# Optimization experiments

Measured on AMD Instinct MI355X. Metric: run time of the kernel, lower is better.

The kernel has to match this reference:

```python
import jax, jax.numpy as jnp
import numpy as np

N = 100000      # nodes
E = 2500000     # edges
DIN, H, DOUT = 3, 32, 4
EPS = 1e-5

def _lin(k, i, o):
    kw, kb = jax.random.split(k)
    lim = 1.0 / np.sqrt(i)
    W = jax.random.uniform(kw, (i, o), jnp.float32, -lim, lim)
    b = jax.random.uniform(kb, (o,), jnp.float32, -lim, lim)
    return W, b

def setup_inputs():
    key = jax.random.key(0)
    ks = jax.random.split(key, 12)
    x = jax.random.normal(ks[0], (N, DIN), jnp.float32)
    edge_index = jax.random.randint(ks[1], (2, E), 0, N, dtype=jnp.int32)
    w_in1, b_in1 = _lin(ks[2], DIN, H)
    w_in2, b_in2 = _lin(ks[3], H, H)
    gamma = jnp.ones((H,), jnp.float32)
    beta = jnp.zeros((H,), jnp.float32)
    wg1, bg1 = _lin(ks[4], H, H)
    wg2, bg2 = _lin(ks[5], H, H)
    wg3, bg3 = _lin(ks[6], H, H)
    wo1, bo1 = _lin(ks[7], H, H)
    wo2, bo2 = _lin(ks[8], H, H)
    wo3, bo3 = _lin(ks[9], H, DOUT)
    return dict(x=x, w_in1=w_in1, b_in1=b_in1, w_in2=w_in2, b_in2=b_in2,
                gamma=gamma, beta=beta,
                wg1=wg1, bg1=bg1, wg2=wg2, bg2=bg2, wg3=wg3, bg3=bg3,
                wo1=wo1, bo1=bo1, wo2=wo2, bo2=bo2, wo3=wo3, bo3=bo3,
                edge_index=edge_index)

def _gcn(h, W, b, src, dst, norm):
    # PyG GCNConv: x' = scatter_add(norm * (xW)[src] -> dst) + bias
    hw = h @ W                                   # [N, H]
    msg = hw[src] * norm[:, None]                # [E+N, H] gather + scale
    out = jax.ops.segment_sum(msg, dst, num_segments=N)
    return out + b

def reference(x, w_in1, b_in1, w_in2, b_in2, gamma, beta,
              wg1, bg1, wg2, bg2, wg3, bg3,
              wo1, bo1, wo2, bo2, wo3, bo3, edge_index):
    leaky = lambda v: jax.nn.leaky_relu(v, 0.01)
    # input MLP
    h = leaky(x @ w_in1 + b_in1)
    h = leaky(h @ w_in2 + b_in2)
    # BatchNorm1d (training-mode batch statistics, biased variance)
    mu = jnp.mean(h, axis=0)
    var = jnp.mean((h - mu) ** 2, axis=0)
    h = (h - mu) * jax.lax.rsqrt(var + EPS) * gamma + beta
    # gcn_norm with self-loops: deg over target index, sym normalization
    loop = jnp.arange(N, dtype=edge_index.dtype)
    src = jnp.concatenate([edge_index[0], loop])
    dst = jnp.concatenate([edge_index[1], loop])
    deg = jax.ops.segment_sum(jnp.ones_like(src, jnp.float32), dst, num_segments=N)
    dis = jax.lax.rsqrt(deg)                     # deg >= 1 due to self-loops
    norm = dis[src] * dis[dst]                   # [E+N]
    h = jax.nn.elu(_gcn(h, wg1, bg1, src, dst, norm))
    h = jax.nn.elu(_gcn(h, wg2, bg2, src, dst, norm))
    h = jax.nn.elu(_gcn(h, wg3, bg3, src, dst, norm))
    # output MLP
    r = leaky(h @ wo1 + bo1)
    r = leaky(r @ wo2 + bo2)
    r = r @ wo3 + bo3                            # [N, 4]
    r = r.at[:, 0].set(jax.nn.sigmoid(r[:, 0]))
    return r
```

## Files before the change

### kernel.cpp

```cpp
#include <hip/hip_runtime.h>
#include <hip/hip_fp16.h>

#define HF 32
#define EPS 1e-5f
#define BSH 7
#define BSZ 128
#define CH  8192
#define SUBCAP 512
#define CAP (8*SUBCAP)

typedef int vi4 __attribute__((ext_vector_type(4)));

__device__ __forceinline__ float leaky(float v){ return fmaxf(v, 0.01f*v); }
__device__ __forceinline__ float elu1(float v){ return v > 0.f ? v : (expf(v)-1.f); }
__device__ __forceinline__ float sigmoidf(float v){ return 1.f/(1.f+expf(-v)); }

__device__ __forceinline__ int4 nt_load_i4(const int* p){
    vi4 v = __builtin_nontemporal_load((const vi4*)p);
    return make_int4(v.x, v.y, v.z, v.w);
}

__device__ __forceinline__ void addrow8(float* a, float4 v){
    const __half2* p = (const __half2*)&v;
#pragma unroll
    for (int k = 0; k < 4; k++){
        float2 f = __half22float2(p[k]);
        a[2*k] += f.x; a[2*k+1] += f.y;
    }
}
__device__ __forceinline__ float4 h2add4f(float4 a, float4 b){
    __half2* pa = (__half2*)&a; __half2* pb = (__half2*)&b;
    float4 r; __half2* pr = (__half2*)&r;
#pragma unroll
    for (int k = 0; k < 4; k++) pr[k] = __hadd2(pa[k], pb[k]);
    return r;
}

union SMem {
    struct {
        float sW1[3*HF]; float sB1[HF]; float sW2[HF*HF]; float sB2[HF];
        float sh[256][33];
    } mlp;
    struct { int lcnt[1024]; int lbase[1024]; int lpos[1024]; } bin;
};

__global__ __launch_bounds__(256)
void k_mlp_bin(const float* __restrict__ x,
               const float* __restrict__ w1, const float* __restrict__ b1,
               const float* __restrict__ w2, const float* __restrict__ b2,
               __half* __restrict__ h, float* __restrict__ stats,
               const int* __restrict__ src, const int* __restrict__ dst,
               int* __restrict__ gfill, int* __restrict__ ep,
               int N, int E, int B, int NB1){
    __shared__ SMem sm;
    int t = threadIdx.x;
    if ((int)blockIdx.x < NB1){
        for (int i = t; i < 3*HF; i += 256) sm.mlp.sW1[i] = w1[i];
        if (t < HF){ sm.mlp.sB1[t] = b1[t]; sm.mlp.sB2[t] = b2[t]; }
        for (int i = t; i < HF*HF; i += 256) sm.mlp.sW2[i] = w2[i];
        __syncthreads();
        int n = blockIdx.x*256 + t;
        float h2[HF];
        if (n < N){
            float x0 = x[(size_t)n*3], x1 = x[(size_t)n*3+1], x2 = x[(size_t)n*3+2];
            float h1[HF];
#pragma unroll
            for (int j = 0; j < HF; j++){
                float v = fmaf(x0, sm.mlp.sW1[j], fmaf(x1, sm.mlp.sW1[HF+j],
                          fmaf(x2, sm.mlp.sW1[2*HF+j], sm.mlp.sB1[j])));
                h1[j] = leaky(v);
            }
#pragma unroll
            for (int j = 0; j < HF; j++){
                float v = sm.mlp.sB2[j];
#pragma unroll
                for (int i = 0; i < HF; i++) v = fmaf(h1[i], sm.mlp.sW2[i*HF+j], v);
                h2[j] = leaky(v);
            }
            float4* hv = (float4*)(h + (size_t)n*HF);
#pragma unroll
            for (int jb = 0; jb < 4; jb++){
                __half2 hh[4];
#pragma unroll
                for (int k = 0; k < 4; k++)
                    hh[k] = __float22half2_rn(make_float2(h2[jb*8+2*k], h2[jb*8+2*k+1]));
                hv[jb] = *(float4*)hh;
            }
        } else {
#pragma unroll
            for (int j = 0; j < HF; j++) h2[j] = 0.f;
        }
#pragma unroll
        for (int j = 0; j < HF; j++) sm.mlp.sh[t][j] = h2[j];
        __syncthreads();
        int f = t & 31, g = t >> 5;
        float s = 0.f, ss = 0.f;
        for (int i = 0; i < 32; i++){
            float v = sm.mlp.sh[g*32 + i][f];
            s += v; ss += v*v;
        }
        __syncthreads();
        sm.mlp.sh[g][f] = s; sm.mlp.sh[8+g][f] = ss;
        __syncthreads();
        if (t < HF){
            float a = 0.f, b = 0.f;
#pragma unroll
            for (int g2 = 0; g2 < 8; g2++){ a += sm.mlp.sh[g2][t]; b += sm.mlp.sh[8+g2][t]; }
            atomicAdd(&stats[t], a);
            atomicAdd(&stats[HF+t], b);
        }
    } else {
        int bid = blockIdx.x - NB1;
        for (int i = t; i < B; i += 256){ sm.bin.lcnt[i] = 0; sm.bin.lpos[i] = 0; }
        __syncthreads();
        int base = bid * CH;
        int xcd = blockIdx.x & 7;
        int dv[16], sv[16];
        for (int half = 0; half < 2; half++){
            int hbase = base + half*4096;
#pragma unroll
            for (int i = 0; i < 16; i++){
                int e = hbase + t + i*256;
                dv[i] = (e < E) ? dst[e] : -1;
                sv[i] = (e < E) ? src[e] : 0;
            }
#pragma unroll
            for (int i = 0; i < 16; i++)
                if (dv[i] >= 0) atomicAdd(&sm.bin.lcnt[dv[i] >> BSH], 1);
            if (half == 0){
            }
            __syncthreads();
            if (half == 0){
            }
        }
        for (int i = t; i < B; i += 256){
            int c = sm.bin.lcnt[i];
            sm.bin.lbase[i] = c ? (i*CAP + xcd*SUBCAP + atomicAdd(&gfill[i*8 + xcd], c)) : 0;
        }
        __syncthreads();
        for (int half = 0; half < 2; half++){
            int hbase = base + half*4096;
#pragma unroll
            for (int i = 0; i < 16; i++){
                int e = hbase + t + i*256;
                if (e < E){
                    int d = dst[e], s = src[e];
                    int bb = d >> BSH;
                    int p = sm.bin.lbase[bb] + atomicAdd(&sm.bin.lpos[bb], 1);
                    ep[p] = (s << BSH) | (d & (BSZ-1));
                }
            }
        }
    }
}

__global__ __launch_bounds__(256)
void k_bucketD(int* __restrict__ ep, const int* __restrict__ gfill,
               int2* __restrict__ rowp2, float* __restrict__ dis, int N, int B){
    __shared__ int sep[CAP];
    __shared__ int lcnt[256], lpre[256], lfill[256], sc[256];
    int b = blockIdx.x, t = threadIdx.x;
    int cx[8], coff[8], cnt = 0;
#pragma unroll
    for (int x = 0; x < 8; x++){ cx[x] = gfill[b*8 + x]; coff[x] = cnt; cnt += cx[x]; }
    lcnt[t] = 0; lfill[t] = 0;
    __syncthreads();
    int base = b*CAP;
#pragma unroll
    for (int x = 0; x < 8; x++)
        for (int j = t; j < cx[x]; j += 256) sep[coff[x] + j] = ep[base + x*SUBCAP + j];
    __syncthreads();
    for (int e = t; e < cnt; e += 256) atomicAdd(&lcnt[sep[e] & (BSZ-1)], 1);
    __syncthreads();
    int v = lcnt[t];
    sc[t] = v; __syncthreads();
    for (int off = 1; off < 256; off <<= 1){
        int u = (t >= off) ? sc[t - off] : 0;
        __syncthreads();
        sc[t] += u;
        __syncthreads();
    }
    int pre = sc[t] - v;
    lpre[t] = pre;
    int n = b*BSZ + t;
    if (t < BSZ && n < N){
        rowp2[n] = make_int2(base + pre, base + pre + v);
        dis[n]   = rsqrtf((float)(v + 1));
    }
    __syncthreads();
    for (int e = t; e < cnt; e += 256){
        int val = sep[e];
        int d = val & (BSZ-1);
        int p = lpre[d] + atomicAdd(&lfill[d], 1);
        ep[base + p] = val >> BSH;
    }
}

__global__ __launch_bounds__(256)
void k_bn_t1(const __half* __restrict__ h, const float* __restrict__ stats,
             const float* __restrict__ gamma, const float* __restrict__ beta,
             const float* __restrict__ W, const float* __restrict__ dis,
             __half* __restrict__ tout, int N){
    __shared__ float sW[HF*HF];
    __shared__ float sh[64][33];
    int tid = threadIdx.x;
    for (int i = tid; i < HF*HF; i += 256) sW[i] = W[i];
    int nib = tid >> 2, l = tid & 3;
    int n = blockIdx.x*64 + nib;
    float hv[8];
    float d = 0.f;
    if (n < N){
        float4 raw = ((const float4*)h)[(size_t)n*4 + l];
        const __half2* p = (const __half2*)&raw;
        float tmp[8];
#pragma unroll
        for (int k = 0; k < 4; k++){
            float2 f2 = __half22float2(p[k]);
            tmp[2*k] = f2.x; tmp[2*k+1] = f2.y;
        }
        d = dis[n];
        float inv = 1.0f / (float)N;
#pragma unroll
        for (int c = 0; c < 8; c++){
            int f = 8*l + c;
            float mu  = stats[f]    * inv;
            float var = stats[HF+f] * inv - mu*mu;
            float rs  = rsqrtf(var + EPS);
            hv[c] = (tmp[c] - mu) * rs * gamma[f] + beta[f];
        }
    } else {
#pragma unroll
        for (int c = 0; c < 8; c++) hv[c] = 0.f;
    }
    __syncthreads();
#pragma unroll
    for (int c = 0; c < 8; c++) sh[nib][8*l + c] = hv[c];
    __syncthreads();
    float o[8] = {0.f,0.f,0.f,0.f,0.f,0.f,0.f,0.f};
#pragma unroll
    for (int i = 0; i < HF; i++){
        float hvv = sh[nib][i];
        float4 w0 = *(const float4*)&sW[i*HF + 8*l];
        float4 w1 = *(const float4*)&sW[i*HF + 8*l + 4];
        o[0] = fmaf(hvv, w0.x, o[0]); o[1] = fmaf(hvv, w0.y, o[1]);
        o[2] = fmaf(hvv, w0.z, o[2]); o[3] = fmaf(hvv, w0.w, o[3]);
        o[4] = fmaf(hvv, w1.x, o[4]); o[5] = fmaf(hvv, w1.y, o[5]);
        o[6] = fmaf(hvv, w1.z, o[6]); o[7] = fmaf(hvv, w1.w, o[7]);
    }
    if (n < N){
        __half2 hh[4];
#pragma unroll
        for (int k = 0; k < 4; k++)
            hh[k] = __float22half2_rn(make_float2(o[2*k]*d, o[2*k+1]*d));
        ((float4*)tout)[(size_t)n*4 + l] = *(float4*)hh;
    }
}

__global__ __launch_bounds__(256)
void k_gather_t(const __half* __restrict__ tin, const int* __restrict__ esrc,
                const int2* __restrict__ rowp2, const float* __restrict__ dis,
                const float* __restrict__ bias, const float* __restrict__ W,
                __half* __restrict__ tout, int N){
    __shared__ float sW[HF*HF];
    __shared__ float sh[64][33];
    int tid = threadIdx.x;
    for (int i = tid; i < HF*HF; i += 256) sW[i] = W[i];
    int nib = tid >> 2, l = tid & 3;
    int n = blockIdx.x*64 + nib;
    float acc[8] = {0.f,0.f,0.f,0.f,0.f,0.f,0.f,0.f};
    float d = 0.f;
    const float4* tv = (const float4*)tin;
    if (n < N){
        addrow8(acc, tv[(size_t)n*4 + l]);
        int2 r = rowp2[n];
        int e = r.x, e1 = r.y;
        while (e < e1 && (e & 3)){ addrow8(acc, tv[(size_t)esrc[e]*4 + l]); e++; }
        for (; e + 7 < e1; e += 8){
            int4 a4 = nt_load_i4(&esrc[e]);
            int4 b4 = nt_load_i4(&esrc[e+4]);
            float4 v0 = tv[(size_t)a4.x*4 + l];
            float4 v1 = tv[(size_t)a4.y*4 + l];
            float4 v2 = tv[(size_t)a4.z*4 + l];
            float4 v3 = tv[(size_t)a4.w*4 + l];
            float4 v4 = tv[(size_t)b4.x*4 + l];
            float4 v5 = tv[(size_t)b4.y*4 + l];
            float4 v6 = tv[(size_t)b4.z*4 + l];
            float4 v7 = tv[(size_t)b4.w*4 + l];
            addrow8(acc, h2add4f(h2add4f(v0, v1), h2add4f(v2, v3)));
            addrow8(acc, h2add4f(h2add4f(v4, v5), h2add4f(v6, v7)));
        }
        for (; e + 3 < e1; e += 4){
            int4 s4 = nt_load_i4(&esrc[e]);
            float4 v0 = tv[(size_t)s4.x*4 + l];
            float4 v1 = tv[(size_t)s4.y*4 + l];
            float4 v2 = tv[(size_t)s4.z*4 + l];
            float4 v3 = tv[(size_t)s4.w*4 + l];
            addrow8(acc, h2add4f(h2add4f(v0, v1), h2add4f(v2, v3)));
        }
        for (; e < e1; e++) addrow8(acc, tv[(size_t)esrc[e]*4 + l]);
        d = dis[n];
#pragma unroll
        for (int c = 0; c < 8; c++)
            acc[c] = elu1(fmaf(d, acc[c], bias[8*l + c]));
    }
    __syncthreads();
#pragma unroll
    for (int c = 0; c < 8; c++) sh[nib][8*l + c] = acc[c];
    __syncthreads();
    float o[8] = {0.f,0.f,0.f,0.f,0.f,0.f,0.f,0.f};
#pragma unroll
    for (int i = 0; i < HF; i++){
        float hvv = sh[nib][i];
        float4 w0 = *(const float4*)&sW[i*HF + 8*l];
        float4 w1 = *(const float4*)&sW[i*HF + 8*l + 4];
        o[0] = fmaf(hvv, w0.x, o[0]); o[1] = fmaf(hvv, w0.y, o[1]);
        o[2] = fmaf(hvv, w0.z, o[2]); o[3] = fmaf(hvv, w0.w, o[3]);
        o[4] = fmaf(hvv, w1.x, o[4]); o[5] = fmaf(hvv, w1.y, o[5]);
        o[6] = fmaf(hvv, w1.z, o[6]); o[7] = fmaf(hvv, w1.w, o[7]);
    }
    if (n < N){
        __half2 hh[4];
#pragma unroll
        for (int k = 0; k < 4; k++)
            hh[k] = __float22half2_rn(make_float2(o[2*k]*d, o[2*k+1]*d));
        ((float4*)tout)[(size_t)n*4 + l] = *(float4*)hh;
    }
}

__global__ __launch_bounds__(256)
void k_gather_out(const __half* __restrict__ tin, const int* __restrict__ esrc,
                  const int2* __restrict__ rowp2, const float* __restrict__ dis,
                  const float* __restrict__ bg3,
                  const float* __restrict__ wo1, const float* __restrict__ bo1,
                  const float* __restrict__ wo2, const float* __restrict__ bo2,
                  const float* __restrict__ wo3, const float* __restrict__ bo3,
                  float* __restrict__ out, int N){
    __shared__ float sW1[HF*HF], sW2[HF*HF], sW3[HF*4];
    __shared__ float sh[64][33], sh2[64][33];
    int tid = threadIdx.x;
    for (int i = tid; i < HF*HF; i += 256){ sW1[i] = wo1[i]; sW2[i] = wo2[i]; }
    if (tid < HF*4) sW3[tid] = wo3[tid];
    int nib = tid >> 2, l = tid & 3;
    int n = blockIdx.x*64 + nib;
    float acc[8] = {0.f,0.f,0.f,0.f,0.f,0.f,0.f,0.f};
    const float4* tv = (const float4*)tin;
    if (n < N){
        addrow8(acc, tv[(size_t)n*4 + l]);
        int2 r = rowp2[n];
        int e = r.x, e1 = r.y;
        while (e < e1 && (e & 3)){ addrow8(acc, tv[(size_t)esrc[e]*4 + l]); e++; }
        for (; e + 7 < e1; e += 8){
            int4 a4 = nt_load_i4(&esrc[e]);
            int4 b4 = nt_load_i4(&esrc[e+4]);
            float4 v0 = tv[(size_t)a4.x*4 + l];
            float4 v1 = tv[(size_t)a4.y*4 + l];
            float4 v2 = tv[(size_t)a4.z*4 + l];
            float4 v3 = tv[(size_t)a4.w*4 + l];
            float4 v4 = tv[(size_t)b4.x*4 + l];
            float4 v5 = tv[(size_t)b4.y*4 + l];
            float4 v6 = tv[(size_t)b4.z*4 + l];
            float4 v7 = tv[(size_t)b4.w*4 + l];
            addrow8(acc, h2add4f(h2add4f(v0, v1), h2add4f(v2, v3)));
            addrow8(acc, h2add4f(h2add4f(v4, v5), h2add4f(v6, v7)));
        }
        for (; e + 3 < e1; e += 4){
            int4 s4 = nt_load_i4(&esrc[e]);
            float4 v0 = tv[(size_t)s4.x*4 + l];
            float4 v1 = tv[(size_t)s4.y*4 + l];
            float4 v2 = tv[(size_t)s4.z*4 + l];
            float4 v3 = tv[(size_t)s4.w*4 + l];
            addrow8(acc, h2add4f(h2add4f(v0, v1), h2add4f(v2, v3)));
        }
        for (; e < e1; e++) addrow8(acc, tv[(size_t)esrc[e]*4 + l]);
        float d = dis[n];
#pragma unroll
        for (int c = 0; c < 8; c++)
            acc[c] = elu1(fmaf(d, acc[c], bg3[8*l + c]));
    }
    __syncthreads();
#pragma unroll
    for (int c = 0; c < 8; c++) sh[nib][8*l + c] = acc[c];
    __syncthreads();
    float o1[8];
#pragma unroll
    for (int c = 0; c < 8; c++) o1[c] = bo1[8*l + c];
#pragma unroll
    for (int i = 0; i < HF; i++){
        float hvv = sh[nib][i];
        float4 w0 = *(const float4*)&sW1[i*HF + 8*l];
        float4 w1 = *(const float4*)&sW1[i*HF + 8*l + 4];
        o1[0] = fmaf(hvv, w0.x, o1[0]); o1[1] = fmaf(hvv, w0.y, o1[1]);
        o1[2] = fmaf(hvv, w0.z, o1[2]); o1[3] = fmaf(hvv, w0.w, o1[3]);
        o1[4] = fmaf(hvv, w1.x, o1[4]); o1[5] = fmaf(hvv, w1.y, o1[5]);
        o1[6] = fmaf(hvv, w1.z, o1[6]); o1[7] = fmaf(hvv, w1.w, o1[7]);
    }
#pragma unroll
    for (int c = 0; c < 8; c++) sh2[nib][8*l + c] = leaky(o1[c]);
    __syncthreads();
    float o2[8];
#pragma unroll
    for (int c = 0; c < 8; c++) o2[c] = bo2[8*l + c];
#pragma unroll
    for (int i = 0; i < HF; i++){
        float hvv = sh2[nib][i];
        float4 w0 = *(const float4*)&sW2[i*HF + 8*l];
        float4 w1 = *(const float4*)&sW2[i*HF + 8*l + 4];
        o2[0] = fmaf(hvv, w0.x, o2[0]); o2[1] = fmaf(hvv, w0.y, o2[1]);
        o2[2] = fmaf(hvv, w0.z, o2[2]); o2[3] = fmaf(hvv, w0.w, o2[3]);
        o2[4] = fmaf(hvv, w1.x, o2[4]); o2[5] = fmaf(hvv, w1.y, o2[5]);
        o2[6] = fmaf(hvv, w1.z, o2[6]); o2[7] = fmaf(hvv, w1.w, o2[7]);
    }
#pragma unroll
    for (int c = 0; c < 8; c++) sh[nib][8*l + c] = leaky(o2[c]);
    __syncthreads();
    if (n < N){
        float v = bo3[l];
#pragma unroll
        for (int i = 0; i < HF; i++) v = fmaf(sh[nib][i], sW3[i*4 + l], v);
        if (l == 0) v = sigmoidf(v);
        out[(size_t)n*4 + l] = v;
    }
}

extern "C" void kernel_launch(void* const* d_in, const int* in_sizes, int n_in,
                              void* d_out, int out_size, void* d_ws, size_t ws_size,
                              hipStream_t stream) {
    const float* x     = (const float*)d_in[0];
    const float* w_in1 = (const float*)d_in[1];
    const float* b_in1 = (const float*)d_in[2];
    const float* w_in2 = (const float*)d_in[3];
    const float* b_in2 = (const float*)d_in[4];
    const float* gamma = (const float*)d_in[5];
    const float* beta  = (const float*)d_in[6];
    const float* wg1   = (const float*)d_in[7];
    const float* bg1   = (const float*)d_in[8];
    const float* wg2   = (const float*)d_in[9];
    const float* bg2   = (const float*)d_in[10];
    const float* wg3   = (const float*)d_in[11];
    const float* bg3   = (const float*)d_in[12];
    const float* wo1   = (const float*)d_in[13];
    const float* bo1   = (const float*)d_in[14];
    const float* wo2   = (const float*)d_in[15];
    const float* bo2   = (const float*)d_in[16];
    const float* wo3   = (const float*)d_in[17];
    const float* bo3   = (const float*)d_in[18];
    const int*   ei    = (const int*)d_in[19];

    int N = in_sizes[0] / 3;
    int E = in_sizes[19] / 2;
    int B = (N + BSZ - 1) >> BSH;

    char* w = (char*)d_ws;
    size_t o = 0;
    auto alloc = [&](size_t bytes){ size_t r = o; o = (o + bytes + 255) & ~(size_t)255; return r; };
    float* stats = (float*)(w + alloc(2*HF*sizeof(float)));
    int*   gfill = (int*)  (w + alloc((size_t)B*8*4));
    size_t zero_bytes = o;
    int2*  rowp2 = (int2*) (w + alloc((size_t)N*8));
    float* dis   = (float*)(w + alloc((size_t)N*4));
    int*   ep    = (int*)  (w + alloc((size_t)B*CAP*4));
    __half* bufH = (__half*)(w + alloc((size_t)N*HF*2));
    __half* tA   = (__half*)(w + alloc((size_t)N*HF*2));
    __half* tB   = (__half*)(w + alloc((size_t)N*HF*2));

    hipMemsetAsync(d_ws, 0, zero_bytes, stream);

    const int* src = ei;
    const int* dst = ei + E;
    int NB1 = (N + 255) / 256;
    int NC  = (E + CH - 1) / CH;
    int GB  = (N + 63) / 64;

    k_mlp_bin<<<NB1 + NC, 256, 0, stream>>>(x, w_in1, b_in1, w_in2, b_in2, bufH, stats,
                                            src, dst, gfill, ep, N, E, B, NB1);
    k_bucketD<<<B, 256, 0, stream>>>(ep, gfill, rowp2, dis, N, B);

    k_bn_t1   <<<GB, 256, 0, stream>>>(bufH, stats, gamma, beta, wg1, dis, tA, N);
    k_gather_t<<<GB, 256, 0, stream>>>(tA, ep, rowp2, dis, bg1, wg2, tB, N);
    k_gather_t<<<GB, 256, 0, stream>>>(tB, ep, rowp2, dis, bg2, wg3, tA, N);
    k_gather_out<<<GB, 256, 0, stream>>>(tA, ep, rowp2, dis, bg3,
                                         wo1, bo1, wo2, bo2, wo3, bo3, (float*)d_out, N);
}
```

Measured before the change: 286.0 us.

## Fuse BatchNorm+first GCN transform into bucket kernel and interleave MLP/bin blocks

Removes the separate k_bn_t1 launch by running BatchNorm and the first 32x32 transform inside k_bucketD. Each bucket block handles the 128 nodes whose degrees it just computed, reads dis from shared memory, and reuses the edge staging buffer through a union. k_mlp_bin now interleaves MLP and binning blocks by block index so both kinds of work are spread across the GPU, and its count pass reads dst directly without register arrays. This saves one launch and a dis reload, but lengthens the bucket kernel and shares the LDS footprint.

```diff
diff --git a/kernel.cpp b/kernel.cpp
--- a/kernel.cpp
+++ b/kernel.cpp
@@ -51,15 +51,21 @@
                __half* __restrict__ h, float* __restrict__ stats,
                const int* __restrict__ src, const int* __restrict__ dst,
                int* __restrict__ gfill, int* __restrict__ ep,
-               int N, int E, int B, int NB1){
+               int N, int E, int B, int NB1, int NC){
     __shared__ SMem sm;
     int t = threadIdx.x;
-    if ((int)blockIdx.x < NB1){
+    int bix = blockIdx.x;
+    bool ismlp; int id;
+    int M = (NC < NB1) ? NC : NB1;
+    if (bix < 2*M){ ismlp = !(bix & 1); id = bix >> 1; }
+    else if (NC < NB1){ ismlp = true;  id = NC  + (bix - 2*NC); }
+    else              { ismlp = false; id = NB1 + (bix - 2*NB1); }
+    if (ismlp){
         for (int i = t; i < 3*HF; i += 256) sm.mlp.sW1[i] = w1[i];
         if (t < HF){ sm.mlp.sB1[t] = b1[t]; sm.mlp.sB2[t] = b2[t]; }
         for (int i = t; i < HF*HF; i += 256) sm.mlp.sW2[i] = w2[i];
         __syncthreads();
-        int n = blockIdx.x*256 + t;
+        int n = id*256 + t;
         float h2[HF];
         if (n < N){
             float x0 = x[(size_t)n*3], x1 = x[(size_t)n*3+1], x2 = x[(size_t)n*3+2];
@@ -110,29 +116,19 @@
             atomicAdd(&stats[HF+t], b);
         }
     } else {
-        int bid = blockIdx.x - NB1;
         for (int i = t; i < B; i += 256){ sm.bin.lcnt[i] = 0; sm.bin.lpos[i] = 0; }
         __syncthreads();
-        int base = bid * CH;
-        int xcd = blockIdx.x & 7;
-        int dv[16], sv[16];
+        int base = id * CH;
+        int xcd = bix & 7;
         for (int half = 0; half < 2; half++){
             int hbase = base + half*4096;
 #pragma unroll
             for (int i = 0; i < 16; i++){
                 int e = hbase + t + i*256;
-                dv[i] = (e < E) ? dst[e] : -1;
-                sv[i] = (e < E) ? src[e] : 0;
-            }
-#pragma unroll
-            for (int i = 0; i < 16; i++)
-                if (dv[i] >= 0) atomicAdd(&sm.bin.lcnt[dv[i] >> BSH], 1);
-            if (half == 0){
-            }
-            __syncthreads();
-            if (half == 0){
-            }
-        }
+                if (e < E) atomicAdd(&sm.bin.lcnt[dst[e] >> BSH], 1);
+            }
+        }
+        __syncthreads();
         for (int i = t; i < B; i += 256){
             int c = sm.bin.lcnt[i];
             sm.bin.lbase[i] = c ? (i*CAP + xcd*SUBCAP + atomicAdd(&gfill[i*8 + xcd], c)) : 0;
@@ -156,28 +152,37 @@
 
 __global__ __launch_bounds__(256)
 void k_bucketD(int* __restrict__ ep, const int* __restrict__ gfill,
-               int2* __restrict__ rowp2, float* __restrict__ dis, int N, int B){
-    __shared__ int sep[CAP];
+               int2* __restrict__ rowp2, float* __restrict__ dis,
+               const __half* __restrict__ h, const float* __restrict__ stats,
+               const float* __restrict__ gamma, const float* __restrict__ beta,
+               const float* __restrict__ W, __half* __restrict__ tout,
+               int N, int B){
+    __shared__ union {
+        int sep[CAP];
+        struct { float sW[HF*HF]; float sh[64][33]; } bn;
+    } u;
     __shared__ int lcnt[256], lpre[256], lfill[256], sc[256];
+    __shared__ float sdis[BSZ];
     int b = blockIdx.x, t = threadIdx.x;
     int cx[8], coff[8], cnt = 0;
 #pragma unroll
     for (int x = 0; x < 8; x++){ cx[x] = gfill[b*8 + x]; coff[x] = cnt; cnt += cx[x]; }
     lcnt[t] = 0; lfill[t] = 0;
+    if (t < BSZ) sdis[t] = 0.f;
     __syncthreads();
     int base = b*CAP;
 #pragma unroll
     for (int x = 0; x < 8; x++)
-        for (int j = t; j < cx[x]; j += 256) sep[coff[x] + j] = ep[base + x*SUBCAP + j];
-    __syncthreads();
-    for (int e = t; e < cnt; e += 256) atomicAdd(&lcnt[sep[e] & (BSZ-1)], 1);
+        for (int j = t; j < cx[x]; j += 256) u.sep[coff[x] + j] = ep[base + x*SUBCAP + j];
+    __syncthreads();
+    for (int e = t; e < cnt; e += 256) atomicAdd(&lcnt[u.sep[e] & (BSZ-1)], 1);
     __syncthreads();
     int v = lcnt[t];
     sc[t] = v; __syncthreads();
     for (int off = 1; off < 256; off <<= 1){
-        int u = (t >= off) ? sc[t - off] : 0;
-        __syncthreads();
-        sc[t] += u;
+        int uu = (t >= off) ? sc[t - off] : 0;
+        __syncthreads();
+        sc[t] += uu;
         __syncthreads();
     }
     int pre = sc[t] - v;
@@ -185,74 +190,68 @@
     int n = b*BSZ + t;
     if (t < BSZ && n < N){
         rowp2[n] = make_int2(base + pre, base + pre + v);
-        dis[n]   = rsqrtf((float)(v + 1));
+        float dv = rsqrtf((float)(v + 1));
+        dis[n] = dv; sdis[t] = dv;
     }
     __syncthreads();
     for (int e = t; e < cnt; e += 256){
-        int val = sep[e];
+        int val = u.sep[e];
         int d = val & (BSZ-1);
         int p = lpre[d] + atomicAdd(&lfill[d], 1);
         ep[base + p] = val >> BSH;
     }
-}
-
-__global__ __launch_bounds__(256)
-void k_bn_t1(const __half* __restrict__ h, const float* __restrict__ stats,
-             const float* __restrict__ gamma, const float* __restrict__ beta,
-             const float* __restrict__ W, const float* __restrict__ dis,
-             __half* __restrict__ tout, int N){
-    __shared__ float sW[HF*HF];
-    __shared__ float sh[64][33];
-    int tid = threadIdx.x;
-    for (int i = tid; i < HF*HF; i += 256) sW[i] = W[i];
-    int nib = tid >> 2, l = tid & 3;
-    int n = blockIdx.x*64 + nib;
-    float hv[8];
-    float d = 0.f;
-    if (n < N){
-        float4 raw = ((const float4*)h)[(size_t)n*4 + l];
-        const __half2* p = (const __half2*)&raw;
-        float tmp[8];
-#pragma unroll
-        for (int k = 0; k < 4; k++){
-            float2 f2 = __half22float2(p[k]);
-            tmp[2*k] = f2.x; tmp[2*k+1] = f2.y;
-        }
-        d = dis[n];
-        float inv = 1.0f / (float)N;
-#pragma unroll
-        for (int c = 0; c < 8; c++){
-            int f = 8*l + c;
-            float mu  = stats[f]    * inv;
-            float var = stats[HF+f] * inv - mu*mu;
-            float rs  = rsqrtf(var + EPS);
-            hv[c] = (tmp[c] - mu) * rs * gamma[f] + beta[f];
-        }
-    } else {
-#pragma unroll
-        for (int c = 0; c < 8; c++) hv[c] = 0.f;
-    }
-    __syncthreads();
-#pragma unroll
-    for (int c = 0; c < 8; c++) sh[nib][8*l + c] = hv[c];
-    __syncthreads();
-    float o[8] = {0.f,0.f,0.f,0.f,0.f,0.f,0.f,0.f};
-#pragma unroll
-    for (int i = 0; i < HF; i++){
-        float hvv = sh[nib][i];
-        float4 w0 = *(const float4*)&sW[i*HF + 8*l];
-        float4 w1 = *(const float4*)&sW[i*HF + 8*l + 4];
-        o[0] = fmaf(hvv, w0.x, o[0]); o[1] = fmaf(hvv, w0.y, o[1]);
-        o[2] = fmaf(hvv, w0.z, o[2]); o[3] = fmaf(hvv, w0.w, o[3]);
-        o[4] = fmaf(hvv, w1.x, o[4]); o[5] = fmaf(hvv, w1.y, o[5]);
-        o[6] = fmaf(hvv, w1.z, o[6]); o[7] = fmaf(hvv, w1.w, o[7]);
-    }
-    if (n < N){
-        __half2 hh[4];
-#pragma unroll
-        for (int k = 0; k < 4; k++)
-            hh[k] = __float22half2_rn(make_float2(o[2*k]*d, o[2*k+1]*d));
-        ((float4*)tout)[(size_t)n*4 + l] = *(float4*)hh;
+    __syncthreads();
+    for (int i = t; i < HF*HF; i += 256) u.bn.sW[i] = W[i];
+    int nib = t >> 2, l = t & 3;
+    float inv = 1.0f / (float)N;
+    for (int half = 0; half < 2; half++){
+        int nl = half*64 + nib;
+        int n2 = b*BSZ + nl;
+        float hv[8];
+        if (n2 < N){
+            float4 raw = ((const float4*)h)[(size_t)n2*4 + l];
+            const __half2* p = (const __half2*)&raw;
+            float tmp[8];
+#pragma unroll
+            for (int k = 0; k < 4; k++){
+                float2 f2 = __half22float2(p[k]);
+                tmp[2*k] = f2.x; tmp[2*k+1] = f2.y;
+            }
+#pragma unroll
+            for (int c = 0; c < 8; c++){
+                int f = 8*l + c;
+                float mu  = stats[f]    * inv;
+                float var = stats[HF+f] * inv - mu*mu;
+                float rs  = rsqrtf(var + EPS);
+                hv[c] = (tmp[c] - mu) * rs * gamma[f] + beta[f];
+            }
+        } else {
+#pragma unroll
+            for (int c = 0; c < 8; c++) hv[c] = 0.f;
+        }
+        __syncthreads();
+#pragma unroll
+        for (int c = 0; c < 8; c++) u.bn.sh[nib][8*l + c] = hv[c];
+        __syncthreads();
+        float o[8] = {0.f,0.f,0.f,0.f,0.f,0.f,0.f,0.f};
+#pragma unroll
+        for (int i = 0; i < HF; i++){
+            float hvv = u.bn.sh[nib][i];
+            float4 w0 = *(const float4*)&u.bn.sW[i*HF + 8*l];
+            float4 w1 = *(const float4*)&u.bn.sW[i*HF + 8*l + 4];
+            o[0] = fmaf(hvv, w0.x, o[0]); o[1] = fmaf(hvv, w0.y, o[1]);
+            o[2] = fmaf(hvv, w0.z, o[2]); o[3] = fmaf(hvv, w0.w, o[3]);
+            o[4] = fmaf(hvv, w1.x, o[4]); o[5] = fmaf(hvv, w1.y, o[5]);
+            o[6] = fmaf(hvv, w1.z, o[6]); o[7] = fmaf(hvv, w1.w, o[7]);
+        }
+        if (n2 < N){
+            float d = sdis[nl];
+            __half2 hh[4];
+#pragma unroll
+            for (int k = 0; k < 4; k++)
+                hh[k] = __float22half2_rn(make_float2(o[2*k]*d, o[2*k+1]*d));
+            ((float4*)tout)[(size_t)n2*4 + l] = *(float4*)hh;
+        }
     }
 }
 
@@ -472,10 +471,10 @@
     int GB  = (N + 63) / 64;
 
     k_mlp_bin<<<NB1 + NC, 256, 0, stream>>>(x, w_in1, b_in1, w_in2, b_in2, bufH, stats,
-                                            src, dst, gfill, ep, N, E, B, NB1);
-    k_bucketD<<<B, 256, 0, stream>>>(ep, gfill, rowp2, dis, N, B);
-
-    k_bn_t1   <<<GB, 256, 0, stream>>>(bufH, stats, gamma, beta, wg1, dis, tA, N);
+                                            src, dst, gfill, ep, N, E, B, NB1, NC);
+    k_bucketD<<<B, 256, 0, stream>>>(ep, gfill, rowp2, dis, bufH, stats,
+                                     gamma, beta, wg1, tA, N, B);
+
     k_gather_t<<<GB, 256, 0, stream>>>(tA, ep, rowp2, dis, bg1, wg2, tB, N);
     k_gather_t<<<GB, 256, 0, stream>>>(tB, ep, rowp2, dis, bg2, wg3, tA, N);
     k_gather_out<<<GB, 256, 0, stream>>>(tA, ep, rowp2, dis, bg3,
```

Result: slower. 303.8 us (+6.2%).
